# Performance work log

Measured on AMD Instinct MI355X. Metric: run time of the kernel, lower is better.

Reference implementation:

```python
import jax, jax.numpy as jnp
import numpy as np

DIM_TIME = 100
NUM_HEAD = 8
DIM_OUT = 256
LN_EPS = 1e-5

# fixed (non-trainable) TimeEncode frequencies: 1 / 10**linspace(0, 9, dim)
_TIME_W = jnp.asarray((1.0 / 10 ** np.linspace(0, 9, DIM_TIME, dtype=np.float32)))


def setup_inputs() -> dict:
    key = jax.random.key(0)
    ks = jax.random.split(key, 16)
    D, E, S = 25000, 500000, 525000
    dn, de = 128, 128
    def lin(k, out_d, in_d):
        return jax.random.normal(k, (out_d, in_d), jnp.float32) * (1.0 / np.sqrt(in_d))
    return {
        "h": jax.random.normal(ks[0], (S, dn), jnp.float32),
        "f": jax.random.normal(ks[1], (E, de), jnp.float32),
        "dt": jax.random.uniform(ks[2], (E,), jnp.float32) * 1000.0,
        "Wq_lin": lin(ks[3], DIM_OUT, dn + DIM_TIME),
        "bq_lin": jnp.zeros((DIM_OUT,), jnp.float32),
        "Wkv_lin": lin(ks[4], DIM_OUT, dn + de + DIM_TIME),
        "bkv_lin": jnp.zeros((DIM_OUT,), jnp.float32),
        "Wq": lin(ks[5], DIM_OUT, DIM_OUT),
        "bq": jnp.zeros((DIM_OUT,), jnp.float32),
        "Wk": lin(ks[6], DIM_OUT, DIM_OUT),
        "bk": jnp.zeros((DIM_OUT,), jnp.float32),
        "Wv": lin(ks[7], DIM_OUT, DIM_OUT),
        "bv": jnp.zeros((DIM_OUT,), jnp.float32),
        "ln_g": jnp.ones((DIM_OUT,), jnp.float32),
        "ln_b": jnp.zeros((DIM_OUT,), jnp.float32),
        "dst": jax.random.randint(ks[8], (E,), 0, D, jnp.int64 if jax.config.jax_enable_x64 else jnp.int32),
    }


def reference(h, f, dt, Wq_lin, bq_lin, Wkv_lin, bkv_lin, Wq, bq, Wk, bk, Wv, bv, ln_g, ln_b, dst):
    E = dst.shape[0]
    D = h.shape[0] - E          # num_dst_nodes; src node D+i is the source of edge i
    H = NUM_HEAD
    dh = DIM_OUT // H

    # TimeEncode (frozen, no grad in original): cos(w * t + 0)
    time_feat = jax.lax.stop_gradient(jnp.cos(dt[:, None] * _TIME_W[None, :]))      # [E, Dt]
    zero_time_feat = jnp.ones((D, DIM_TIME), h.dtype)                               # cos(0) = 1

    # Q from dst nodes; K/V from src-neighbor nodes + edge feat + time feat
    Q_ori = jnp.concatenate([h[:D], zero_time_feat], axis=1) @ Wq_lin.T + bq_lin    # [D, dout]
    K_ori = jnp.concatenate([h[D:], f, time_feat], axis=1) @ Wkv_lin.T + bkv_lin    # [E, dout]

    # augmented edge set: E real edges + D self-loops (dst attends to itself)
    Qfull = jnp.concatenate([Q_ori[dst], Q_ori], axis=0)                            # [E+D, dout]
    KVfull = jnp.concatenate([K_ori, Q_ori], axis=0)                                # [E+D, dout]

    Qh = (Qfull @ Wq.T + bq).reshape(-1, H, dh)
    Kh = (KVfull @ Wk.T + bk).reshape(-1, H, dh)
    Vh = (KVfull @ Wv.T + bv).reshape(-1, H, dh)

    scores = jax.nn.leaky_relu(jnp.sum(Qh * Kh, axis=2), negative_slope=0.2)        # [E+D, H]

    dst_all = jnp.concatenate([dst, jnp.arange(D, dtype=dst.dtype)], axis=0)        # [E+D]

    # segment (edge) softmax over destination nodes; every dst has a self-loop
    seg_max = jnp.full((D, H), -jnp.inf, scores.dtype).at[dst_all].max(scores)
    ex = jnp.exp(scores - seg_max[dst_all])
    seg_sum = jnp.zeros((D, H), scores.dtype).at[dst_all].add(ex)
    att = ex / seg_sum[dst_all]                                                     # [E+D, H]

    # weighted scatter-sum aggregation (copy_u/sum over the augmented block)
    Vw = (Vh * att[:, :, None]).reshape(-1, DIM_OUT)                                # [E+D, dout]
    agg = jnp.zeros((D, DIM_OUT), h.dtype).at[dst_all].add(Vw)                      # [D, dout]

    rst = jax.nn.relu(agg)                                                          # dropout = identity (eval)
    mu = jnp.mean(rst, axis=-1, keepdims=True)
    var = jnp.mean((rst - mu) ** 2, axis=-1, keepdims=True)
    return (rst - mu) * jax.lax.rsqrt(var + LN_EPS) * ln_g + ln_b
```

## Files before the change

kernel.cpp:

```cpp
#include <hip/hip_runtime.h>
#include <cstdint>
#include <cstddef>


typedef _Float16 f16_t;
typedef _Float16 f16x8 __attribute__((ext_vector_type(8)));
typedef _Float16 f16x4 __attribute__((ext_vector_type(4)));
typedef float    f32x4 __attribute__((ext_vector_type(4)));

#define MFMA16(a, b, c) __builtin_amdgcn_mfma_f32_16x16x32_f16(a, b, c, 0, 0, 0)

#define BARRIER()                                         \
  do {                                                    \
    asm volatile("s_waitcnt lgkmcnt(0)" ::: "memory");    \
    __builtin_amdgcn_sched_barrier(0);                    \
    __builtin_amdgcn_s_barrier();                         \
    __builtin_amdgcn_sched_barrier(0);                    \
  } while (0)

static __device__ __forceinline__ f32x4 zero4() {
  f32x4 v; v[0] = 0.f; v[1] = 0.f; v[2] = 0.f; v[3] = 0.f; return v;
}

#define TIMEW_LOG2 (-0.30199346317157837f)

__global__ void k_ph(const float* __restrict__ wq_lin,
                     const float* __restrict__ bq_lin,
                     const float* __restrict__ wq,
                     const float* __restrict__ wk,
                     const float* __restrict__ wv,
                     const int* __restrict__ dst,
                     f16_t* __restrict__ wq1,
                     f16_t* __restrict__ w3,
                     float* __restrict__ bqe,
                     int* __restrict__ rs, int E) {
  const int b = blockIdx.x;
  if (b >= 898) {
    int e = (b - 898) * 256 + threadIdx.x;
    if (e < E) atomicAdd(&rs[dst[e] + 1], 1);
    return;
  }
  int i = b * 256 + threadIdx.x;
  if (i < 32768) {
    int o = i >> 7, k = i & 127;
    wq1[i] = (f16_t)wq_lin[o * 228 + k];
  } else if (i < 229376) {
    int j = i - 32768;
    int r = j >> 8, k = j & 255;
    const float* src = (r < 256) ? wq : ((r < 512) ? wk : wv);
    w3[j] = (f16_t)src[(r & 255) * 256 + k];
  } else if (i < 229632) {
    int o = i - 229376;
    float s = bq_lin[o];
    for (int j = 0; j < 100; ++j) s += wq_lin[o * 228 + 128 + j];
    bqe[o] = s;
  }
}

__global__ __launch_bounds__(384) void k_wcomp(
    const float* __restrict__ wkv_lin, const float* __restrict__ bkv,
    const float* __restrict__ wk, const float* __restrict__ bk,
    const float* __restrict__ wv, const float* __restrict__ bv,
    f16_t* __restrict__ weffp, float* __restrict__ beff) {
  __shared__ float wrow[256];
  const int oc = blockIdx.x;
  const float* src = (oc < 256) ? (wk + (size_t)oc * 256)
                                : (wv + (size_t)(oc - 256) * 256);
  const int t = threadIdx.x;
  if (t < 256) wrow[t] = src[t];
  __syncthreads();

  float acc = 0.f;
  if (t < 356) {
#pragma unroll 4
    for (int m = 0; m < 256; ++m) acc += wrow[m] * wkv_lin[(size_t)m * 356 + t];
  }
  int kc = t >> 5, g = (t >> 3) & 3, j = t & 7;
  weffp[(size_t)kc * 16384 + g * 4096 + oc * 8 + j] = (f16_t)acc;

  if (t == 0) {
    float b = (oc < 256) ? bk[oc] : bv[oc - 256];
    for (int m = 0; m < 256; ++m) b += wrow[m] * bkv[m];
    beff[oc] = b;
  }
}

__global__ __launch_bounds__(1024) void k_scan(int* __restrict__ rs,
                                               int* __restrict__ cur, int D) {
  __shared__ int wsum[16];
  __shared__ int srun;
  const int t = threadIdx.x, lane = t & 63, wv = t >> 6;
  if (t == 0) srun = 0;
  __syncthreads();
  for (int base = 0; base < D; base += 1024) {
    const int i = base + t;
    const int c = (i < D) ? rs[i + 1] : 0;
    int x = c;
#pragma unroll
    for (int off = 1; off < 64; off <<= 1) {
      int y = __shfl_up(x, off);
      if (lane >= off) x += y;
    }
    if (lane == 63) wsum[wv] = x;
    __syncthreads();
    if (wv == 0 && lane < 16) {
      int w = wsum[lane];
#pragma unroll
      for (int off = 1; off < 16; off <<= 1) {
        int y = __shfl_up(w, off);
        if (lane >= off) w += y;
      }
      wsum[lane] = w;
    }
    __syncthreads();
    const int incl = x + ((wv > 0) ? wsum[wv - 1] : 0);
    const int run = srun;
    __syncthreads();
    if (i < D) {
      cur[i] = run + incl - c;
      rs[i + 1] = run + incl;
    }
    if (t == 1023) srun = run + incl;
    __syncthreads();
  }
}

__global__ void k_sentinel(float* __restrict__ o, int n) {
  int i = blockIdx.x * 256 + threadIdx.x;
  if (i < n) o[i] = 1e30f;
}

__global__ __launch_bounds__(512) void k_sq(
    const float* __restrict__ h, const float* __restrict__ bqe,
    const float* __restrict__ bq, const float* __restrict__ bk,
    const float* __restrict__ bv, const f16_t* __restrict__ wq1,
    const f16_t* __restrict__ w3, float* __restrict__ qhd,
    f16_t* __restrict__ khs, f16_t* __restrict__ vhs, int D,
    const int* __restrict__ dst, int* __restrict__ cur,
    int* __restrict__ csr, int* __restrict__ dstc, int E, int nq) {
  __shared__ f16_t sm[64 * 256];
  if ((int)blockIdx.x >= nq) {
    int e = ((int)blockIdx.x - nq) * 512 + (int)threadIdx.x;
    if (e < E) {
      int d = dst[e];
      int pos = atomicAdd(&cur[d], 1);
      csr[pos] = e;
      dstc[pos] = d;
    }
    return;
  }
  f16_t* xs = sm;
  f16_t* ks = sm;
  const int tid = threadIdx.x;
  const int dbase = blockIdx.x * 64;

  {
    const int r = tid >> 3, q = tid & 7;
    const int dd = min(dbase + r, D - 1);
    const int sw = r & 7;
    const float* p = h + (size_t)dd * 128 + q * 16;
#pragma unroll
    for (int u = 0; u < 2; ++u) {
      float4 v0 = *(const float4*)(p + u * 8);
      float4 v1 = *(const float4*)(p + u * 8 + 4);
      f16x8 w8;
      w8[0] = (f16_t)v0.x; w8[1] = (f16_t)v0.y; w8[2] = (f16_t)v0.z; w8[3] = (f16_t)v0.w;
      w8[4] = (f16_t)v1.x; w8[5] = (f16_t)v1.y; w8[6] = (f16_t)v1.z; w8[7] = (f16_t)v1.w;
      *(f16x8*)&xs[r * 128 + (((2 * q + u) ^ sw) << 3)] = w8;
    }
  }
  __syncthreads();

  const int lane = tid & 63;
  const int wv_ = tid >> 6;
  const int m16 = lane & 15;
  const int g = lane >> 4;

  f32x4 acc1[4][2];
#pragma unroll
  for (int mt = 0; mt < 4; ++mt)
#pragma unroll
    for (int nt = 0; nt < 2; ++nt) acc1[mt][nt] = zero4();

#pragma unroll
  for (int kt = 0; kt < 4; ++kt) {
    f16x8 a[4];
#pragma unroll
    for (int mt = 0; mt < 4; ++mt) {
      int row = mt * 16 + m16;
      a[mt] = *(const f16x8*)&xs[row * 128 + ((((kt << 2) + g) ^ (row & 7)) << 3)];
    }
#pragma unroll
    for (int nt = 0; nt < 2; ++nt) {
      int col = wv_ * 32 + nt * 16 + m16;
      f16x8 b = *(const f16x8*)&wq1[(size_t)col * 128 + (kt << 5) + (g << 3)];
#pragma unroll
      for (int mt = 0; mt < 4; ++mt) acc1[mt][nt] = MFMA16(a[mt], b, acc1[mt][nt]);
    }
  }
  __syncthreads();

#pragma unroll
  for (int nt = 0; nt < 2; ++nt) {
    int col = wv_ * 32 + nt * 16 + m16;
    float bias = bqe[col];
#pragma unroll
    for (int mt = 0; mt < 4; ++mt)
#pragma unroll
      for (int j = 0; j < 4; ++j) {
        int row = mt * 16 + (g << 2) + j;
        ks[row * 256 + ((((col >> 3) ^ (row & 7)) << 3)) + (col & 7)] =
            (f16_t)(acc1[mt][nt][j] + bias);
      }
  }
  __syncthreads();

#pragma unroll
  for (int p = 0; p < 3; ++p) {
    const f16_t* wsec = w3 + ((size_t)p << 16);
    const float* bsec = (p == 0) ? bq : ((p == 1) ? bk : bv);
    f32x4 acc[4][2];
#pragma unroll
    for (int mt = 0; mt < 4; ++mt)
#pragma unroll
      for (int nt = 0; nt < 2; ++nt) acc[mt][nt] = zero4();
#pragma unroll
    for (int kt = 0; kt < 8; ++kt) {
      f16x8 a[4];
#pragma unroll
      for (int mt = 0; mt < 4; ++mt) {
        int row = mt * 16 + m16;
        a[mt] = *(const f16x8*)&ks[row * 256 + ((((kt << 2) + g) ^ (row & 7)) << 3)];
      }
#pragma unroll
      for (int nt = 0; nt < 2; ++nt) {
        int col = wv_ * 32 + nt * 16 + m16;
        f16x8 b = *(const f16x8*)&wsec[(size_t)col * 256 + (kt << 5) + (g << 3)];
#pragma unroll
        for (int mt = 0; mt < 4; ++mt) acc[mt][nt] = MFMA16(a[mt], b, acc[mt][nt]);
      }
    }
#pragma unroll
    for (int nt = 0; nt < 2; ++nt) {
      int col = wv_ * 32 + nt * 16 + m16;
      float bias = bsec[col];
#pragma unroll
      for (int mt = 0; mt < 4; ++mt)
#pragma unroll
        for (int j = 0; j < 4; ++j) {
          int row = mt * 16 + (g << 2) + j;
          int dd = dbase + row;
          if (dd < D) {
            float val = acc[mt][nt][j] + bias;
            if (p == 0)
              qhd[(size_t)dd * 256 + col] = val;
            else if (p == 1)
              khs[(size_t)dd * 256 + col] = (f16_t)val;
            else
              vhs[(size_t)dd * 256 + col] = (f16_t)val;
          }
        }
    }
  }
}

__global__ __launch_bounds__(512, 4) void k_kv(
    const float* __restrict__ h, const float* __restrict__ f,
    const float* __restrict__ dt, const f16_t* __restrict__ weffp,
    const float* __restrict__ beff, const int* __restrict__ csr,
    const int* __restrict__ dstc, const float* __restrict__ qhd,
    float* __restrict__ agg, int D, int E) {
  __shared__ __align__(16) unsigned char smem[40960];

  const int tid = threadIdx.x;
  const int pbase = blockIdx.x * 64;
  const int row = tid >> 3, q = tid & 7;
  const int lane = tid & 63, wn = tid >> 6;
  const int m16 = lane & 15, g = lane >> 4;

  const int pclamp = min(pbase + row, E - 1);
  const int ec = csr[pclamp];
  const float dtv = dt[ec];
  const float* hrow = h + (size_t)(D + ec) * 128 + q * 4;
  const float* frow = f + (size_t)ec * 128 + q * 4;

  auto stageA = [&](int buf, int sub, float4 v) {
    f16x4 w;
    w[0] = (f16_t)v.x; w[1] = (f16_t)v.y; w[2] = (f16_t)v.z; w[3] = (f16_t)v.w;
    *(f16x4*)(smem + buf * 20480 + sub * 5120 + row * 80 + q * 8) = w;
  };
  const f16_t* wb = weffp + (size_t)g * 4096 + ((size_t)(wn * 64 + m16) << 3);
  auto gldB = [&](int kc, f16x8* d) {
    const f16_t* pB = wb + (size_t)kc * 16384;
#pragma unroll
    for (int n = 0; n < 4; ++n) d[n] = *(const f16x8*)(pB + n * 128);
  };

  f32x4 acc[4][4];
#pragma unroll
  for (int mt = 0; mt < 4; ++mt)
#pragma unroll
    for (int n = 0; n < 4; ++n) acc[mt][n] = zero4();

  auto doChunk = [&](int kc, const f16x8* bbuf) {
    const unsigned char* Ac =
        smem + (((kc >> 2) == 1) ? 20480 : 0) + (kc & 3) * 5120;
#pragma unroll
    for (int mt = 0; mt < 4; ++mt) {
      f16x8 afr = *(const f16x8*)(Ac + (mt * 16 + m16) * 80 + g * 16);
#pragma unroll
      for (int n = 0; n < 4; ++n) acc[mt][n] = MFMA16(afr, bbuf[n], acc[mt][n]);
    }
  };

  float4 hv[4], fv[4];
#pragma unroll
  for (int s = 0; s < 4; ++s) hv[s] = *(const float4*)(hrow + s * 32);
#pragma unroll
  for (int s = 0; s < 4; ++s) fv[s] = *(const float4*)(frow + s * 32);
  f16x8 bb0[4], bb1[4];
  gldB(0, bb0);
  gldB(1, bb1);
#pragma unroll
  for (int s = 0; s < 4; ++s) stageA(0, s, hv[s]);
#pragma unroll
  for (int s = 0; s < 4; ++s) stageA(1, s, fv[s]);
  BARRIER();

  doChunk(0, bb0); gldB(2, bb0);
  doChunk(1, bb1); gldB(3, bb1);
  doChunk(2, bb0); gldB(4, bb0);
  doChunk(3, bb1);
  BARRIER();

#pragma unroll
  for (int s = 0; s < 4; ++s) {
    float4 a;
#pragma unroll
    for (int j = 0; j < 4; ++j) {
      int cc = s * 32 + q * 4 + j;
      ((float*)&a)[j] =
          (cc < 100) ? __cosf(dtv * exp2f(TIMEW_LOG2 * (float)cc)) : 0.f;
    }
    stageA(0, s, a);
  }
  gldB(5, bb1); doChunk(4, bb0);
  gldB(6, bb0); doChunk(5, bb1);
  gldB(7, bb1); doChunk(6, bb0);
  gldB(8, bb0); doChunk(7, bb1);
  BARRIER();

  gldB(9, bb1);  doChunk(8, bb0);
  gldB(10, bb0); doChunk(9, bb1);
  gldB(11, bb1); doChunk(10, bb0);
  doChunk(11, bb1);
  BARRIER();

  f16_t* ep    = (f16_t*)smem;
  float* ee_s  = (float*)(smem + 33792);
  int*   dst_s = (int*)(smem + 35840);

  if (wn < 4) {
#pragma unroll
    for (int n = 0; n < 4; ++n) {
      const int c256 = wn * 64 + n * 16 + m16;
      const float bias = beff[c256];
#pragma unroll
      for (int mt = 0; mt < 4; ++mt)
#pragma unroll
        for (int j = 0; j < 4; ++j) {
          const int r2 = mt * 16 + (g << 2) + j;
          ep[r2 * 264 + c256] = (f16_t)(acc[mt][n][j] + bias);
        }
    }
  }
  BARRIER();

  {
    const int r2 = tid >> 3, hp = tid & 7;
    const int p2 = pbase + r2;
    float eev = 0.f;
    if (p2 < E) {
      const int de = dstc[p2];
      const float* qp = qhd + (size_t)de * 256 + hp * 32;
      const f16_t* kp = ep + r2 * 264 + hp * 32;
      float s = 0.f;
#pragma unroll
      for (int jj = 0; jj < 32; jj += 4) {
        float4 qv = *(const float4*)(qp + jj);
        f16x4 kv = *(const f16x4*)(kp + jj);
        s += qv.x * (float)kv[0] + qv.y * (float)kv[1] +
             qv.z * (float)kv[2] + qv.w * (float)kv[3];
      }
      s = (s > 0.f) ? s : 0.2f * s;
      eev = __expf(s);
    }
    ee_s[r2 * 8 + hp] = eev;
    if (hp == 0) dst_s[r2] = dstc[min(p2, E - 1)];
  }
  BARRIER();

  if (wn >= 4) {
#pragma unroll
    for (int n = 0; n < 4; ++n) {
      const int c256 = (wn - 4) * 64 + n * 16 + m16;
      const float bias = beff[256 + c256];
#pragma unroll
      for (int mt = 0; mt < 4; ++mt)
#pragma unroll
        for (int j = 0; j < 4; ++j) {
          const int r2 = mt * 16 + (g << 2) + j;
          ep[r2 * 264 + c256] = (f16_t)(acc[mt][n][j] + bias);
        }
    }
  }
  BARRIER();

  {
    const int half = tid >> 8;
    const int c = tid & 255;
    const int hd = c >> 5;
    const int r0 = half * 32;
    float accv = 0.f;
    int cur_d = dst_s[r0];
#pragma unroll 8
    for (int r = r0; r < r0 + 32; ++r) {
      int dd = dst_s[r];
      if (dd != cur_d) {
        atomicAdd(&agg[(size_t)cur_d * 264 + c], accv);
        accv = 0.f;
        cur_d = dd;
      }
      accv = fmaf(ee_s[r * 8 + hd], (float)ep[r * 264 + c], accv);
    }
    atomicAdd(&agg[(size_t)cur_d * 264 + c], accv);
  }
  if (tid < 16) {
    const int half = tid >> 3, hd = tid & 7;
    const int r0 = half * 32;
    float accv = 0.f;
    int cur_d = dst_s[r0];
#pragma unroll 8
    for (int r = r0; r < r0 + 32; ++r) {
      int dd = dst_s[r];
      if (dd != cur_d) {
        atomicAdd(&agg[(size_t)cur_d * 264 + 256 + hd], accv);
        accv = 0.f;
        cur_d = dd;
      }
      accv += ee_s[r * 8 + hd];
    }
    atomicAdd(&agg[(size_t)cur_d * 264 + 256 + hd], accv);
  }
}

__global__ __launch_bounds__(256) void k_fin(
    const float* __restrict__ qhd, const f16_t* __restrict__ khs,
    const f16_t* __restrict__ vhs, const float* __restrict__ agg,
    const float* __restrict__ lng, const float* __restrict__ lnb,
    float* __restrict__ out, int D) {
  const int lane = threadIdx.x & 63;
  const int d = blockIdx.x * 4 + (threadIdx.x >> 6);
  if (d >= D) return;
  const int c0 = lane * 4;
  const int hd = lane >> 3;

  float4 av = *(const float4*)(agg + (size_t)d * 264 + c0);
  float den = agg[(size_t)d * 264 + 256 + hd];

  {
    float4 qv = *(const float4*)(qhd + (size_t)d * 256 + c0);
    f16x4 ku = *(const f16x4*)(khs + (size_t)d * 256 + c0);
    f16x4 vu = *(const f16x4*)(vhs + (size_t)d * 256 + c0);
    float s = qv.x * (float)ku[0] + qv.y * (float)ku[1] +
              qv.z * (float)ku[2] + qv.w * (float)ku[3];
    s += __shfl_xor(s, 1); s += __shfl_xor(s, 2); s += __shfl_xor(s, 4);
    s = (s > 0.f) ? s : 0.2f * s;
    float ee = __expf(s);
    den += ee;
    av.x = fmaf(ee, (float)vu[0], av.x);
    av.y = fmaf(ee, (float)vu[1], av.y);
    av.z = fmaf(ee, (float)vu[2], av.z);
    av.w = fmaf(ee, (float)vu[3], av.w);
  }

  float x0 = fmaxf(av.x / den, 0.f), x1 = fmaxf(av.y / den, 0.f);
  float x2 = fmaxf(av.z / den, 0.f), x3 = fmaxf(av.w / den, 0.f);

  float s1 = x0 + x1 + x2 + x3;
#pragma unroll
  for (int m = 1; m < 64; m <<= 1) s1 += __shfl_xor(s1, m);
  float mu = s1 * (1.f / 256.f);
  float d0 = x0 - mu, d1 = x1 - mu, d2 = x2 - mu, d3 = x3 - mu;
  float s2 = d0 * d0 + d1 * d1 + d2 * d2 + d3 * d3;
#pragma unroll
  for (int m = 1; m < 64; m <<= 1) s2 += __shfl_xor(s2, m);
  float rstd = rsqrtf(s2 * (1.f / 256.f) + 1e-5f);

  float4 gg = *(const float4*)(lng + c0);
  float4 bb = *(const float4*)(lnb + c0);
  float4 o;
  o.x = d0 * rstd * gg.x + bb.x;
  o.y = d1 * rstd * gg.y + bb.y;
  o.z = d2 * rstd * gg.z + bb.z;
  o.w = d3 * rstd * gg.w + bb.w;
  *(float4*)(out + (size_t)d * 256 + c0) = o;
}

extern "C" void kernel_launch(void* const* d_in, const int* in_sizes, int n_in,
                              void* d_out, int out_size, void* d_ws,
                              size_t ws_size, hipStream_t stream) {
  const float* h       = (const float*)d_in[0];
  const float* f       = (const float*)d_in[1];
  const float* dt      = (const float*)d_in[2];
  const float* wq_lin  = (const float*)d_in[3];
  const float* bq_lin  = (const float*)d_in[4];
  const float* wkv_lin = (const float*)d_in[5];
  const float* bkv_lin = (const float*)d_in[6];
  const float* wq      = (const float*)d_in[7];
  const float* bq      = (const float*)d_in[8];
  const float* wk      = (const float*)d_in[9];
  const float* bk      = (const float*)d_in[10];
  const float* wv      = (const float*)d_in[11];
  const float* bv      = (const float*)d_in[12];
  const float* lng     = (const float*)d_in[13];
  const float* lnb     = (const float*)d_in[14];
  const int*   dst     = (const int*)d_in[15];

  const int S = in_sizes[0] / 128;
  const int E = in_sizes[2];
  const int D = S - E;
  float* out = (float*)d_out;

  char* p = (char*)d_ws;
  size_t off = 0;
  auto take = [&](size_t bytes) -> char* {
    char* r = p + off;
    off += (bytes + 255) & ~(size_t)255;
    return r;
  };
  f16_t* wq1   = (f16_t*)take((size_t)32768 * 2);
  f16_t* w3    = (f16_t*)take((size_t)196608 * 2);
  float* bqe   = (float*)take((size_t)256 * 4);
  f16_t* weffp = (f16_t*)take((size_t)196608 * 2);
  float* beff  = (float*)take((size_t)512 * 4);
  float* qhd   = (float*)take((size_t)D * 256 * 4);
  f16_t* khs   = (f16_t*)take((size_t)D * 256 * 2);
  f16_t* vhs   = (f16_t*)take((size_t)D * 256 * 2);
  float* agg   = (float*)take((size_t)D * 264 * 4);
  int*   rs    = (int*)  take((size_t)(D + 1) * 4);
  int*   cur   = (int*)  take((size_t)D * 4);
  int*   csr   = (int*)  take((size_t)E * 4);
  int*   dstc  = (int*)  take((size_t)E * 4);

  if (off > ws_size) {
    k_sentinel<<<(out_size + 255) / 256, 256, 0, stream>>>(out, out_size);
    return;
  }

  const int nq = (D + 63) / 64;
  const int nsc = (E + 511) / 512;

  hipMemsetAsync(agg, 0, (size_t)((char*)rs - (char*)agg) + (size_t)(D + 1) * 4,
                 stream);
  k_ph<<<898 + (E + 255) / 256, 256, 0, stream>>>(wq_lin, bq_lin, wq, wk, wv,
                                                  dst, wq1, w3, bqe, rs, E);
  k_wcomp<<<512, 384, 0, stream>>>(wkv_lin, bkv_lin, wk, bk, wv, bv, weffp,
                                   beff);
  k_scan<<<1, 1024, 0, stream>>>(rs, cur, D);
  k_sq<<<nq + nsc, 512, 0, stream>>>(h, bqe, bq, bk, bv, wq1, w3, qhd, khs,
                                     vhs, D, dst, cur, csr, dstc, E, nq);
  k_kv<<<(E + 63) / 64, 512, 0, stream>>>(h, f, dt, weffp, beff, csr, dstc,
                                          qhd, agg, D, E);
  k_fin<<<(D + 3) / 4, 256, 0, stream>>>(qhd, khs, vhs, agg, lng, lnb, out, D);
}
```

Before: 503.7 us.

## Prefetch Q into registers, split K/V LDS staging, batch weight composition rows

```diff
diff --git a/kernel.cpp b/kernel.cpp
--- a/kernel.cpp
+++ b/kernel.cpp
@@ -62,25 +62,37 @@
     const float* __restrict__ wk, const float* __restrict__ bk,
     const float* __restrict__ wv, const float* __restrict__ bv,
     f16_t* __restrict__ weffp, float* __restrict__ beff) {
-  __shared__ float wrow[256];
-  const int oc = blockIdx.x;
-  const float* src = (oc < 256) ? (wk + (size_t)oc * 256)
-                                : (wv + (size_t)(oc - 256) * 256);
+  __shared__ float wrow[8][256];
+  const int ocb = blockIdx.x * 8;
   const int t = threadIdx.x;
-  if (t < 256) wrow[t] = src[t];
+  for (int i = t; i < 8 * 256; i += 384) {
+    int j = i >> 8, m = i & 255;
+    int oc = ocb + j;
+    const float* src = (oc < 256) ? (wk + (size_t)oc * 256)
+                                  : (wv + (size_t)(oc - 256) * 256);
+    wrow[j][m] = src[m];
+  }
   __syncthreads();
 
-  float acc = 0.f;
+  float acc[8];
+#pragma unroll
+  for (int j = 0; j < 8; ++j) acc[j] = 0.f;
   if (t < 356) {
-#pragma unroll 4
-    for (int m = 0; m < 256; ++m) acc += wrow[m] * wkv_lin[(size_t)m * 356 + t];
-  }
-  int kc = t >> 5, g = (t >> 3) & 3, j = t & 7;
-  weffp[(size_t)kc * 16384 + g * 4096 + oc * 8 + j] = (f16_t)acc;
-
-  if (t == 0) {
+    for (int m = 0; m < 256; ++m) {
+      float x = wkv_lin[(size_t)m * 356 + t];
+#pragma unroll
+      for (int j = 0; j < 8; ++j) acc[j] = fmaf(wrow[j][m], x, acc[j]);
+    }
+  }
+  int kc = t >> 5, g = (t >> 3) & 3, jj = t & 7;
+#pragma unroll
+  for (int j = 0; j < 8; ++j)
+    weffp[(size_t)kc * 16384 + g * 4096 + (ocb + j) * 8 + jj] = (f16_t)acc[j];
+
+  if (t < 8) {
+    int oc = ocb + t;
     float b = (oc < 256) ? bk[oc] : bv[oc - 256];
-    for (int m = 0; m < 256; ++m) b += wrow[m] * bkv[m];
+    for (int m = 0; m < 256; ++m) b += wrow[t][m] * bkv[m];
     beff[oc] = b;
   }
 }
@@ -270,7 +282,7 @@
     const float* __restrict__ beff, const int* __restrict__ csr,
     const int* __restrict__ dstc, const float* __restrict__ qhd,
     float* __restrict__ agg, int D, int E) {
-  __shared__ __align__(16) unsigned char smem[40960];
+  __shared__ __align__(16) unsigned char smem[70144];
 
   const int tid = threadIdx.x;
   const int pbase = blockIdx.x * 64;
@@ -313,19 +325,29 @@
     }
   };
 
-  float4 hv[4], fv[4];
-#pragma unroll
-  for (int s = 0; s < 4; ++s) hv[s] = *(const float4*)(hrow + s * 32);
-#pragma unroll
-  for (int s = 0; s < 4; ++s) fv[s] = *(const float4*)(frow + s * 32);
   f16x8 bb0[4], bb1[4];
   gldB(0, bb0);
   gldB(1, bb1);
-#pragma unroll
-  for (int s = 0; s < 4; ++s) stageA(0, s, hv[s]);
-#pragma unroll
-  for (int s = 0; s < 4; ++s) stageA(1, s, fv[s]);
+  {
+    float4 hv[4], fv[4];
+#pragma unroll
+    for (int s = 0; s < 4; ++s) hv[s] = *(const float4*)(hrow + s * 32);
+#pragma unroll
+    for (int s = 0; s < 4; ++s) fv[s] = *(const float4*)(frow + s * 32);
+#pragma unroll
+    for (int s = 0; s < 4; ++s) stageA(0, s, hv[s]);
+#pragma unroll
+    for (int s = 0; s < 4; ++s) stageA(1, s, fv[s]);
+  }
   BARRIER();
+
+  const int deq = dstc[pclamp];
+  float4 qpre[8];
+  {
+    const float* qp = qhd + (size_t)deq * 256 + q * 32;
+#pragma unroll
+    for (int jj = 0; jj < 8; ++jj) qpre[jj] = *(const float4*)(qp + jj * 4);
+  }
 
   doChunk(0, bb0); gldB(2, bb0);
   doChunk(1, bb1); gldB(3, bb1);
@@ -356,15 +378,20 @@
   doChunk(11, bb1);
   BARRIER();
 
-  f16_t* ep    = (f16_t*)smem;
-  float* ee_s  = (float*)(smem + 33792);
-  int*   dst_s = (int*)(smem + 35840);
-
-  if (wn < 4) {
+  f16_t* epk   = (f16_t*)smem;
+  f16_t* epv   = (f16_t*)(smem + 34048);
+  float* ee_s  = (float*)(smem + 67840);
+  int*   dst_s = (int*)(smem + 69888);
+
+  {
+    const int half = wn >> 2;
+    f16_t* ep = half ? epv : epk;
+    const float* bofs = beff + half * 256;
+    const int wl = wn & 3;
 #pragma unroll
     for (int n = 0; n < 4; ++n) {
-      const int c256 = wn * 64 + n * 16 + m16;
-      const float bias = beff[c256];
+      const int c256 = wl * 64 + n * 16 + m16;
+      const float bias = bofs[c256];
 #pragma unroll
       for (int mt = 0; mt < 4; ++mt)
 #pragma unroll
@@ -381,38 +408,19 @@
     const int p2 = pbase + r2;
     float eev = 0.f;
     if (p2 < E) {
-      const int de = dstc[p2];
-      const float* qp = qhd + (size_t)de * 256 + hp * 32;
-      const f16_t* kp = ep + r2 * 264 + hp * 32;
+      const f16_t* kp = epk + r2 * 264 + hp * 32;
       float s = 0.f;
 #pragma unroll
-      for (int jj = 0; jj < 32; jj += 4) {
-        float4 qv = *(const float4*)(qp + jj);
-        f16x4 kv = *(const f16x4*)(kp + jj);
-        s += qv.x * (float)kv[0] + qv.y * (float)kv[1] +
-             qv.z * (float)kv[2] + qv.w * (float)kv[3];
+      for (int jj = 0; jj < 8; ++jj) {
+        f16x4 kv = *(const f16x4*)(kp + jj * 4);
+        s += qpre[jj].x * (float)kv[0] + qpre[jj].y * (float)kv[1] +
+             qpre[jj].z * (float)kv[2] + qpre[jj].w * (float)kv[3];
       }
       s = (s > 0.f) ? s : 0.2f * s;
       eev = __expf(s);
     }
     ee_s[r2 * 8 + hp] = eev;
-    if (hp == 0) dst_s[r2] = dstc[min(p2, E - 1)];
-  }
-  BARRIER();
-
-  if (wn >= 4) {
-#pragma unroll
-    for (int n = 0; n < 4; ++n) {
-      const int c256 = (wn - 4) * 64 + n * 16 + m16;
-      const float bias = beff[256 + c256];
-#pragma unroll
-      for (int mt = 0; mt < 4; ++mt)
-#pragma unroll
-        for (int j = 0; j < 4; ++j) {
-          const int r2 = mt * 16 + (g << 2) + j;
-          ep[r2 * 264 + c256] = (f16_t)(acc[mt][n][j] + bias);
-        }
-    }
+    if (hp == 0) dst_s[r2] = deq;
   }
   BARRIER();
 
@@ -431,7 +439,7 @@
         accv = 0.f;
         cur_d = dd;
       }
-      accv = fmaf(ee_s[r * 8 + hd], (float)ep[r * 264 + c], accv);
+      accv = fmaf(ee_s[r * 8 + hd], (float)epv[r * 264 + c], accv);
     }
     atomicAdd(&agg[(size_t)cur_d * 264 + c], accv);
   }
@@ -565,8 +573,8 @@
                  stream);
   k_ph<<<898 + (E + 255) / 256, 256, 0, stream>>>(wq_lin, bq_lin, wq, wk, wv,
                                                   dst, wq1, w3, bqe, rs, E);
-  k_wcomp<<<512, 384, 0, stream>>>(wkv_lin, bkv_lin, wk, bk, wv, bv, weffp,
-                                   beff);
+  k_wcomp<<<64, 384, 0, stream>>>(wkv_lin, bkv_lin, wk, bk, wv, bv, weffp,
+                                  beff);
   k_scan<<<1, 1024, 0, stream>>>(rs, cur, D);
   k_sq<<<nq + nsc, 512, 0, stream>>>(h, bqe, bq, bk, bv, wq1, w3, qhd, khs,
                                      vhs, D, dst, cur, csr, dstc, E, nq);
```

Result: no change. 508.5 us (+1.0%).
